# Kernel tuning notes

Hardware: AMD Instinct MI355X
Metric: run time of the kernel (lower is better)

## Reference

```python
import jax, jax.numpy as jnp
import numpy as np

N, E, IN_C, H, C1, OUT_C, B = 10000, 100000, 256, 6, 128, 128, 64
EPS = 1e-5
NEG_SLOPE = 0.2


def gat_conv(x, src, dst, W, att_s, att_d, bias):
    # x: [N, F_in]; W: [F_in, H*C]; att_s/att_d: [H, C]; bias: [H*C]
    n, h, c = x.shape[0], att_s.shape[0], att_s.shape[1]
    hx = (x @ W).reshape(n, h, c)                    # [N,H,C]
    a_s = jnp.einsum('nhc,hc->nh', hx, att_s)        # [N,H]
    a_d = jnp.einsum('nhc,hc->nh', hx, att_d)
    e = jax.nn.leaky_relu(a_s[src] + a_d[dst], NEG_SLOPE)   # [E,H]
    # segment softmax over incoming edges of each dst node
    m = jax.ops.segment_max(e, dst, num_segments=n)
    e = jnp.exp(e - m[dst])
    s = jax.ops.segment_sum(e, dst, num_segments=n)
    alpha = e / s[dst]                               # [E,H]
    msg = hx[src] * alpha[:, :, None]                # [E,H,C]
    out = jax.ops.segment_sum(msg, dst, num_segments=n)
    return out.reshape(n, h * c) + bias


def batch_norm(x, gamma, beta):
    mu = jnp.mean(x, axis=0)
    var = jnp.var(x, axis=0)  # biased, as torch BN uses for normalization
    return (x - mu) * jax.lax.rsqrt(var + EPS) * gamma + beta


def setup_inputs() -> dict:
    key = jax.random.key(0)
    ks = jax.random.split(key, 12)
    def xavier(k, shape):
        fan_in, fan_out = shape[0], shape[1]
        lim = np.sqrt(6.0 / (fan_in + fan_out))
        return jax.random.uniform(k, shape, jnp.float32, -lim, lim)
    inp = {}
    inp['input_feature'] = jax.random.normal(ks[0], (N, IN_C), jnp.float32)
    inp['input_adj'] = jax.random.randint(ks[1], (2, E), 0, N, jnp.int64)
    inp['ibatch'] = (jnp.arange(N, dtype=jnp.int64) * B) // N  # sorted graph ids, all B graphs covered
    # conv1: in -> H*C1
    inp['W1'] = xavier(ks[2], (IN_C, H * C1))
    inp['att_s1'] = xavier(ks[3], (H, C1)) * 0.1
    inp['att_d1'] = xavier(ks[4], (H, C1)) * 0.1
    inp['b1'] = jnp.zeros((H * C1,), jnp.float32)
    inp['g1'] = jnp.ones((H * C1,), jnp.float32)
    inp['be1'] = jnp.zeros((H * C1,), jnp.float32)
    # conv2: H*C1 -> H*OUT_C
    inp['W2'] = xavier(ks[5], (H * C1, H * OUT_C))
    inp['att_s2'] = xavier(ks[6], (H, OUT_C)) * 0.1
    inp['att_d2'] = xavier(ks[7], (H, OUT_C)) * 0.1
    inp['b2'] = jnp.zeros((H * OUT_C,), jnp.float32)
    inp['g2'] = jnp.ones((H * OUT_C,), jnp.float32)
    inp['be2'] = jnp.zeros((H * OUT_C,), jnp.float32)
    # gcn_linear: H*OUT_C -> OUT_C
    inp['lin_W'] = xavier(ks[8], (H * OUT_C, OUT_C))
    inp['lin_b'] = jnp.zeros((OUT_C,), jnp.float32)
    return inp


def reference(input_feature, input_adj, ibatch, W1, att_s1, att_d1, b1, g1, be1,
              W2, att_s2, att_d2, b2, g2, be2, lin_W, lin_b):
    # add self loops (PyG GATConv default)
    loops = jnp.arange(N, dtype=input_adj.dtype)
    src = jnp.concatenate([input_adj[0], loops])
    dst = jnp.concatenate([input_adj[1], loops])
    x = gat_conv(input_feature, src, dst, W1, att_s1, att_d1, b1)
    x = batch_norm(jax.nn.relu(x), g1, be1)
    x = gat_conv(x, src, dst, W2, att_s2, att_d2, b2)
    x = batch_norm(jax.nn.relu(x), g2, be2)
    x = x @ lin_W + lin_b                             # [N, OUT_C]
    # global max pool over nodes of each graph
    return jax.ops.segment_max(x, ibatch, num_segments=B)
```

## Files before the change

kernel.cpp:

```cpp
#include <hip/hip_runtime.h>

#define NN 10000
#define MP 10112
#define EE 100000
#define ETOT 110000
#define INC 256
#define HH 6
#define CC 128
#define FF 768
#define BB 64
#define BN_EPS 1e-5f

typedef unsigned short ushort_t;
typedef unsigned int uint_t;
typedef __attribute__((ext_vector_type(8))) short bf16x8;
typedef __attribute__((ext_vector_type(4))) float f32x4;
#define AS1 __attribute__((address_space(1)))
#define AS3 __attribute__((address_space(3)))

__device__ __forceinline__ unsigned fenc(float v){
  unsigned u = __float_as_uint(v);
  return (u & 0x80000000u) ? ~u : (u | 0x80000000u);
}
__device__ __forceinline__ float fdec(unsigned u){
  return (u & 0x80000000u) ? __uint_as_float(u & 0x7FFFFFFFu) : __uint_as_float(~u);
}

__device__ __forceinline__ ushort_t f2bf(float v){
  unsigned u = __float_as_uint(v);
  u += 0x7FFFu + ((u >> 16) & 1u);
  return (ushort_t)(u >> 16);
}
__device__ __forceinline__ float bf_lo(uint_t u){ return __uint_as_float(u << 16); }
__device__ __forceinline__ float bf_hi(uint_t u){ return __uint_as_float(u & 0xFFFF0000u); }

__device__ __forceinline__ float bn_scale(const float* sums, const float* sumsq,
                                          const float* g, int k){
  float mu  = sums[k] * (1.f/NN);
  float var = sumsq[k] * (1.f/NN) - mu*mu;
  return g[k] * rsqrtf(var + BN_EPS);
}

#define PREP_CNT 430
#define PREP_TR  (24*8)
#define PREP_CVT 2500
__global__ __launch_bounds__(256) void prep(const int* __restrict__ adj, int* __restrict__ deg,
                                            const float* __restrict__ W1, ushort_t* __restrict__ W1t,
                                            const float* __restrict__ feat, ushort_t* __restrict__ featB){
  __shared__ ushort_t tile[32][33];
  int bid = blockIdx.x, tid = threadIdx.x;
  if(bid < PREP_CNT){
    int k = bid*256 + tid;
    if(k < ETOT){
      int d = (k < EE) ? adj[EE + k] : (k - EE);
      atomicAdd(deg + d, 1);
    }
  } else if(bid < PREP_CNT + PREP_TR){
    int b = bid - PREP_CNT;
    int nb = (b % 24)*32, kb = (b / 24)*32;
    int tx = tid & 31, ty = tid >> 5;
    #pragma unroll
    for(int r = ty; r < 32; r += 8)
      tile[tx][r] = f2bf(W1[(size_t)(kb + r)*FF + nb + tx]);
    __syncthreads();
    #pragma unroll
    for(int r = ty; r < 32; r += 8)
      W1t[(size_t)(nb + r)*INC + kb + tx] = tile[r][tx];
  } else {
    int i = (bid - PREP_CNT - PREP_TR)*256 + tid;
    float4 v = ((const float4*)feat)[i];
    ushort4 o;
    o.x = f2bf(v.x); o.y = f2bf(v.y); o.z = f2bf(v.z); o.w = f2bf(v.w);
    ((ushort4*)featB)[i] = o;
  }
}

__global__ __launch_bounds__(1024) void scan_deg(const int* __restrict__ deg,
                                                 int* __restrict__ row_start,
                                                 int* __restrict__ pos){
  __shared__ int wsum[16];
  __shared__ int wexcl[16];
  __shared__ int carry, ctot;
  int t = threadIdx.x, wave = t >> 6, lane = t & 63;
  if(t == 0) carry = 0;
  __syncthreads();
  for(int base = 0; base < NN; base += 1024){
    int i = base + t;
    int v = (i < NN) ? deg[i] : 0;
    int s = v;
    #pragma unroll
    for(int off = 1; off < 64; off <<= 1){ int x = __shfl_up(s, off); if(lane >= off) s += x; }
    if(lane == 63) wsum[wave] = s;
    __syncthreads();
    if(t < 16){
      int ws = wsum[t], sc = ws;
      #pragma unroll
      for(int off = 1; off < 16; off <<= 1){ int x = __shfl_up(sc, off); if(t >= off) sc += x; }
      wexcl[t] = sc - ws;
      if(t == 15) ctot = sc;
    }
    __syncthreads();
    int c = carry;
    if(i < NN){ int excl = c + wexcl[wave] + s - v; row_start[i] = excl; pos[i] = excl; }
    __syncthreads();
    if(t == 0) carry = c + ctot;
  }
  __syncthreads();
  if(t == 0) row_start[NN] = carry;
}

__global__ __launch_bounds__(256) void scatter_edges(const int* __restrict__ adj,
                                                     int* __restrict__ pos,
                                                     int* __restrict__ csr_src){
  int k = blockIdx.x*256 + threadIdx.x;
  if(k >= ETOT) return;
  int s, d;
  if(k < EE){ s = adj[k]; d = adj[EE + k]; } else { s = k - EE; d = s; }
  int i = atomicAdd(pos + d, 1);
  csr_src[i] = s;
}

__global__ __launch_bounds__(256) void wfold(const float* __restrict__ W,
                                             int K, int N,
                                             const float* __restrict__ sums,
                                             const float* __restrict__ sumsq,
                                             const float* __restrict__ g,
                                             const float* __restrict__ be,
                                             const float* __restrict__ base,
                                             ushort_t* __restrict__ Wt,
                                             float* __restrict__ biasOut){
  __shared__ ushort_t tile[32][33];
  int nT = (K >> 5)*(N >> 5);
  int bid = blockIdx.x, tid = threadIdx.x;
  if(bid < nT){
    int nb = (bid % (N >> 5))*32, kb = (bid / (N >> 5))*32;
    int tx = tid & 31, ty = tid >> 5;
    #pragma unroll
    for(int r = ty; r < 32; r += 8){
      int k = kb + r;
      tile[tx][r] = f2bf(W[(size_t)k*N + nb + tx] * bn_scale(sums, sumsq, g, k));
    }
    __syncthreads();
    #pragma unroll
    for(int r = ty; r < 32; r += 8)
      Wt[(size_t)(nb + r)*K + kb + tx] = tile[r][tx];
  } else {
    int b = bid - nT;
    int oChunks = (N + 255) >> 8;
    int kc = b / oChunks, oc = b % oChunks;
    int o = oc*256 + tid;
    if(o >= N) return;
    int k0 = kc*64, k1 = k0 + 64;
    float s = 0.f;
    for(int k = k0; k < k1; k++){
      float mu = sums[k] * (1.f/NN);
      float sc = bn_scale(sums, sumsq, g, k);
      s = fmaf(be[k] - mu*sc, W[(size_t)k*N + o], s);
    }
    if(k0 == 0 && base) s += base[o];
    atomicAdd(biasOut + o, s);
  }
}

#define CTS 136
__global__ __launch_bounds__(256) void gemm_bt(const ushort_t* __restrict__ A,
                                               const ushort_t* __restrict__ Bt,
                                               ushort_t* __restrict__ Cb,
                                               int M, int N, int K,
                                               const float* __restrict__ bias,
                                               const float* __restrict__ atts,
                                               const float* __restrict__ attd,
                                               float* __restrict__ a_s,
                                               float* __restrict__ a_d,
                                               const int* __restrict__ ibatch,
                                               unsigned* __restrict__ outEnc){
  __shared__ ushort_t smem[8704];
  __shared__ unsigned smax[2*CC];
  __shared__ int s_split;
  ushort_t* As = smem;
  ushort_t* Bs = smem + 4096;
  int tid = threadIdx.x;
  int bm = blockIdx.y*128, bn = blockIdx.x*128;
  int w = tid >> 6, lane = tid & 63;
  int wr = (w >> 1)*64, wc = (w & 1)*64;
  int quad = lane >> 4, l15 = lane & 15;

  f32x4 acc[4][4];
  #pragma unroll
  for(int i=0;i<4;i++)
    #pragma unroll
    for(int j=0;j<4;j++) acc[i][j] = (f32x4){0.f,0.f,0.f,0.f};

  int ch0 = tid, ch1 = tid + 256;
  int ar0 = ch0 >> 2, ac0 = (ch0 & 3) << 3;
  int ar1 = ch1 >> 2, ac1 = (ch1 & 3) << 3;
  const ushort_t* Ag0 = A + (size_t)(bm + ar0)*K + ac0;
  const ushort_t* Ag1 = A + (size_t)(bm + ar1)*K + ac1;
  const ushort_t* Bg0 = Bt + (size_t)(bn + ar0)*K + ac0;
  const ushort_t* Bg1 = Bt + (size_t)(bn + ar1)*K + ac1;

  for(int k0 = 0; k0 < K; k0 += 32){
    __builtin_amdgcn_global_load_lds((const AS1 uint_t*)(Ag0 + k0),
                                     (AS3 uint_t*)(As + ch0*8), 16, 0, 0);
    __builtin_amdgcn_global_load_lds((const AS1 uint_t*)(Ag1 + k0),
                                     (AS3 uint_t*)(As + ch1*8), 16, 0, 0);
    __builtin_amdgcn_global_load_lds((const AS1 uint_t*)(Bg0 + k0),
                                     (AS3 uint_t*)(Bs + ch0*8), 16, 0, 0);
    __builtin_amdgcn_global_load_lds((const AS1 uint_t*)(Bg1 + k0),
                                     (AS3 uint_t*)(Bs + ch1*8), 16, 0, 0);
    __syncthreads();

    bf16x8 a[4], b[4];
    #pragma unroll
    for(int i=0;i<4;i++) a[i] = *(const bf16x8*)&As[(wr + i*16 + l15)*32 + quad*8];
    #pragma unroll
    for(int j=0;j<4;j++) b[j] = *(const bf16x8*)&Bs[(wc + j*16 + l15)*32 + quad*8];
    #pragma unroll
    for(int i=0;i<4;i++)
      #pragma unroll
      for(int j=0;j<4;j++)
        acc[i][j] = __builtin_amdgcn_mfma_f32_16x16x32_bf16(a[i], b[j], acc[i][j], 0, 0, 0);
    __syncthreads();
  }

  int h = bn >> 7;
  float bv4[4];
  #pragma unroll
  for(int j=0;j<4;j++){
    int gc = bn + wc + j*16 + l15;
    bv4[j] = bias ? bias[gc] : 0.f;
  }

  if(outEnc){
    if(tid == 0) s_split = bm + 128;
    for(int q = tid; q < 2*CC; q += 256) smax[q] = 0u;
    __syncthreads();
    if(tid < 127){
      int r1 = bm + tid + 1;
      if(r1 < M && ibatch[r1] != ibatch[r1 - 1]) s_split = r1;
    }
    __syncthreads();
    int gsplit = s_split;
    float pm[2][4];
    #pragma unroll
    for(int s2=0;s2<2;s2++)
      #pragma unroll
      for(int j=0;j<4;j++) pm[s2][j] = -__builtin_inff();
    #pragma unroll
    for(int i=0;i<4;i++){
      #pragma unroll
      for(int r=0;r<4;r++){
        int gr = bm + wr + i*16 + quad*4 + r;
        if(gr < M){
          int slot = (gr >= gsplit);
          #pragma unroll
          for(int j=0;j<4;j++)
            pm[slot][j] = fmaxf(pm[slot][j], acc[i][j][r] + bv4[j]);
        }
      }
    }
    #pragma unroll
    for(int s2=0;s2<2;s2++)
      #pragma unroll
      for(int j=0;j<4;j++){
        if(pm[s2][j] > -__builtin_inff())
          atomicMax(&smax[s2*CC + wc + j*16 + l15], fenc(pm[s2][j]));
      }
    __syncthreads();
    if(tid < 2*CC){
      unsigned v = smax[tid];
      if(v){
        int slot = tid >> 7, c = tid & 127;
        int g = ibatch[slot ? gsplit : bm];
        atomicMax(outEnc + g*CC + c, v);
      }
    }
  } else {
    ushort_t* Ct = smem;
    int myp = w >> 1;
    #pragma unroll
    for(int p=0;p<2;p++){
      if(myp == p){
        #pragma unroll
        for(int i=0;i<4;i++)
          #pragma unroll
          for(int r=0;r<4;r++){
            int row = i*16 + quad*4 + r;
            #pragma unroll
            for(int j=0;j<4;j++)
              Ct[row*CTS + wc + j*16 + l15] = f2bf(acc[i][j][r] + bv4[j]);
          }
      }
      __syncthreads();
      #pragma unroll
      for(int k=0;k<4;k++){
        int c = tid + 256*k;
        int row = c >> 4, o16 = c & 15;
        int gr = bm + p*64 + row;
        if(gr < M)
          *(uint4*)(Cb + (size_t)gr*N + bn + o16*8) = *(const uint4*)&Ct[row*CTS + o16*8];
      }
      if(atts){
        int row = tid >> 2, qtr = tid & 3;
        int gr = bm + p*64 + row;
        float sp = 0.f, dp = 0.f;
        const float2* asp = (const float2*)(atts + h*CC) + qtr*16;
        const float2* adp = (const float2*)(attd + h*CC) + qtr*16;
        const uint_t* cr = (const uint_t*)smem + ((row*CTS) >> 1) + qtr*16;
        #pragma unroll
        for(int c2=0;c2<16;c2++){
          uint_t u = cr[c2];
          float2 a2 = asp[c2], d2 = adp[c2];
          sp = fmaf(bf_lo(u), a2.x, fmaf(bf_hi(u), a2.y, sp));
          dp = fmaf(bf_lo(u), d2.x, fmaf(bf_hi(u), d2.y, dp));
        }
        sp += __shfl_xor(sp, 1); sp += __shfl_xor(sp, 2);
        dp += __shfl_xor(dp, 1); dp += __shfl_xor(dp, 2);
        if(qtr == 0 && gr < M){ a_s[gr*6 + h] = sp; a_d[gr*6 + h] = dp; }
      }
      __syncthreads();
    }
  }
}

__global__ __launch_bounds__(384) void aggregate(const ushort_t* __restrict__ hx,
                                                 const float* __restrict__ a_s,
                                                 const float* __restrict__ a_d,
                                                 const int* __restrict__ row_start,
                                                 const int* __restrict__ csr_src,
                                                 const float* __restrict__ bias,
                                                 ushort_t* __restrict__ y){
  int n = blockIdx.x, t = threadIdx.x, h = t >> 6;
  int e0 = row_start[n], e1 = row_start[n+1];
  float adv = a_d[n*6 + h];
  float a0 = 0.f, a1 = 0.f, wsum = 0.f;
  int i = e0;
  for(; i + 8 <= e1; i += 8){
    int s[8]; float wv[8]; uint_t u[8];
    #pragma unroll
    for(int q=0;q<8;q++) s[q] = csr_src[i+q];
    #pragma unroll
    for(int q=0;q<8;q++) wv[q] = a_s[s[q]*6 + h];
    #pragma unroll
    for(int q=0;q<8;q++) u[q] = ((const uint_t*)(hx + (size_t)s[q]*FF))[t];
    #pragma unroll
    for(int q=0;q<8;q++){
      float v = wv[q] + adv;
      v = v > 0.f ? v : 0.2f * v;
      float wq = __expf(v);
      wsum += wq;
      a0 = fmaf(wq, bf_lo(u[q]), a0); a1 = fmaf(wq, bf_hi(u[q]), a1);
    }
  }
  if(i + 4 <= e1){
    int s[4]; float wv[4]; uint_t u[4];
    #pragma unroll
    for(int q=0;q<4;q++) s[q] = csr_src[i+q];
    #pragma unroll
    for(int q=0;q<4;q++) wv[q] = a_s[s[q]*6 + h];
    #pragma unroll
    for(int q=0;q<4;q++) u[q] = ((const uint_t*)(hx + (size_t)s[q]*FF))[t];
    #pragma unroll
    for(int q=0;q<4;q++){
      float v = wv[q] + adv;
      v = v > 0.f ? v : 0.2f * v;
      float wq = __expf(v);
      wsum += wq;
      a0 = fmaf(wq, bf_lo(u[q]), a0); a1 = fmaf(wq, bf_hi(u[q]), a1);
    }
    i += 4;
  }
  for(; i < e1; i++){
    int s = csr_src[i];
    float v = a_s[s*6 + h] + adv;
    v = v > 0.f ? v : 0.2f * v;
    float wq = __expf(v);
    wsum += wq;
    uint_t u = ((const uint_t*)(hx + (size_t)s*FF))[t];
    a0 = fmaf(wq, bf_lo(u), a0); a1 = fmaf(wq, bf_hi(u), a1);
  }
  float inv = 1.f/wsum;
  float2 bv = ((const float2*)bias)[t];
  float v0 = a0*inv + bv.x;
  float v1 = a1*inv + bv.y;
  v0 = v0 > 0.f ? v0 : 0.f;
  v1 = v1 > 0.f ? v1 : 0.f;
  uint_t p = (uint_t)f2bf(v0) | ((uint_t)f2bf(v1) << 16);
  ((uint_t*)(y + (size_t)n*FF))[t] = p;
}

__global__ __launch_bounds__(384) void bn_stats(const ushort_t* __restrict__ y,
                                                float* __restrict__ sums,
                                                float* __restrict__ sumsq){
  int t = threadIdx.x;
  float s0=0.f,s1=0.f,q0=0.f,q1=0.f;
  for(int n = blockIdx.x; n < NN; n += gridDim.x){
    uint_t u = ((const uint_t*)(y + (size_t)n*FF))[t];
    float lo = bf_lo(u), hi = bf_hi(u);
    s0 += lo; q0 += lo*lo;
    s1 += hi; q1 += hi*hi;
  }
  atomicAdd(sums + 2*t,     s0); atomicAdd(sumsq + 2*t,     q0);
  atomicAdd(sums + 2*t + 1, s1); atomicAdd(sumsq + 2*t + 1, q1);
}

__global__ __launch_bounds__(256) void decode_out(const unsigned* __restrict__ outEnc,
                                                  float* __restrict__ out){
  int i = blockIdx.x*256 + threadIdx.x;
  if(i < BB*CC) out[i] = fdec(outEnc[i]);
}

extern "C" void kernel_launch(void* const* d_in, const int* in_sizes, int n_in,
                              void* d_out, int out_size, void* d_ws, size_t ws_size,
                              hipStream_t stream){
  const float* feat  = (const float*)d_in[0];
  const int*   adj   = (const int*)d_in[1];
  const int*   ibatch= (const int*)d_in[2];
  const float* W1    = (const float*)d_in[3];
  const float* atts1 = (const float*)d_in[4];
  const float* attd1 = (const float*)d_in[5];
  const float* b1    = (const float*)d_in[6];
  const float* g1    = (const float*)d_in[7];
  const float* be1   = (const float*)d_in[8];
  const float* W2    = (const float*)d_in[9];
  const float* atts2 = (const float*)d_in[10];
  const float* attd2 = (const float*)d_in[11];
  const float* b2    = (const float*)d_in[12];
  const float* g2    = (const float*)d_in[13];
  const float* be2   = (const float*)d_in[14];
  const float* linW  = (const float*)d_in[15];
  const float* linb  = (const float*)d_in[16];
  float* out = (float*)d_out;

  size_t off = 0;
  auto alloc = [&](size_t bytes) -> void* {
    void* p = (char*)d_ws + off;
    off += (bytes + 255) & ~(size_t)255;
    return p;
  };
  size_t zoff0 = off;
  int*      deg     = (int*)alloc((size_t)NN*4);
  float*    sumsA   = (float*)alloc((size_t)2*FF*4);
  float*    sumsB   = (float*)alloc((size_t)2*FF*4);
  float*    bias2p  = (float*)alloc((size_t)FF*4);
  float*    biasLp  = (float*)alloc((size_t)CC*4);
  unsigned* outEnc  = (unsigned*)alloc((size_t)BB*CC*4);
  size_t zbytes = off - zoff0;
  ushort_t* hx      = (ushort_t*)alloc((size_t)NN*FF*2);
  ushort_t* yB      = (ushort_t*)alloc((size_t)MP*FF*2);
  ushort_t* featB   = (ushort_t*)alloc((size_t)MP*INC*2);
  ushort_t* W1t     = (ushort_t*)alloc((size_t)FF*INC*2);
  ushort_t* W2t     = (ushort_t*)alloc((size_t)FF*FF*2);
  ushort_t* linWt   = (ushort_t*)alloc((size_t)CC*FF*2);
  float*    a_s     = (float*)alloc((size_t)NN*6*4);
  float*    a_d     = (float*)alloc((size_t)NN*6*4);
  int*      row_start=(int*)alloc((size_t)(NN+1)*4);
  int*      pos     = (int*)alloc((size_t)NN*4);
  int*      csr_src = (int*)alloc((size_t)ETOT*4);

  const int EB = (ETOT + 255)/256;

  hipMemsetAsync((char*)d_ws + zoff0, 0, zbytes, stream);

  prep<<<PREP_CNT + PREP_TR + PREP_CVT,256,0,stream>>>(adj, deg, W1, W1t, feat, featB);
  scan_deg<<<1,1024,0,stream>>>(deg, row_start, pos);
  scatter_edges<<<EB,256,0,stream>>>(adj, pos, csr_src);

  gemm_bt<<<dim3(FF/128, MP/128),256,0,stream>>>(featB, W1t, hx, NN, FF, INC,
                                                 nullptr, atts1, attd1, a_s, a_d, nullptr, nullptr);
  aggregate<<<NN,384,0,stream>>>(hx, a_s, a_d, row_start, csr_src, b1, yB);
  bn_stats<<<256,384,0,stream>>>(yB, sumsA, sumsA + FF);

  wfold<<<(FF/32)*(FF/32) + (FF/64)*3,256,0,stream>>>(W2, FF, FF, sumsA, sumsA + FF, g1, be1,
                                                      nullptr, W2t, bias2p);
  gemm_bt<<<dim3(FF/128, MP/128),256,0,stream>>>(yB, W2t, hx, NN, FF, FF,
                                                 bias2p, atts2, attd2, a_s, a_d, nullptr, nullptr);
  aggregate<<<NN,384,0,stream>>>(hx, a_s, a_d, row_start, csr_src, b2, yB);
  bn_stats<<<256,384,0,stream>>>(yB, sumsB, sumsB + FF);

  wfold<<<(FF/32)*(CC/32) + (FF/64)*1,256,0,stream>>>(linW, FF, CC, sumsB, sumsB + FF, g2, be2,
                                                      linb, linWt, biasLp);
  gemm_bt<<<dim3(CC/128, MP/128),256,0,stream>>>(yB, linWt, nullptr, NN, CC, FF,
                                                 biasLp, nullptr, nullptr, nullptr, nullptr,
                                                 ibatch, outEnc);
  decode_out<<<(BB*CC+255)/256,256,0,stream>>>(outEnc, out);
}
```

Before: 327.1 us.

## Split-K the final linear GEMM and move max-pooling into a separate kernel

The final linear layer (N x 768 by 768 x 128) used to launch only 79 blocks with fused max-pool. It now runs a split-K GEMM with 4 K-chunks and 64-row tiles (632 blocks), writing fp32 partial sums to a workspace. A new pool kernel then sums the partials, adds the bias and does the per-graph segment max with atomics. This aims to fill more CUs, at the cost of an extra launch and about 20 MB of partial-sum writes and reads.

```diff
diff --git a/kernel.cpp b/kernel.cpp
--- a/kernel.cpp
+++ b/kernel.cpp
@@ -171,12 +171,8 @@
                                                const float* __restrict__ atts,
                                                const float* __restrict__ attd,
                                                float* __restrict__ a_s,
-                                               float* __restrict__ a_d,
-                                               const int* __restrict__ ibatch,
-                                               unsigned* __restrict__ outEnc){
+                                               float* __restrict__ a_d){
   __shared__ ushort_t smem[8704];
-  __shared__ unsigned smax[2*CC];
-  __shared__ int s_split;
   ushort_t* As = smem;
   ushort_t* Bs = smem + 4096;
   int tid = threadIdx.x;
@@ -230,97 +226,133 @@
     int gc = bn + wc + j*16 + l15;
     bv4[j] = bias ? bias[gc] : 0.f;
   }
-
-  if(outEnc){
-    if(tid == 0) s_split = bm + 128;
-    for(int q = tid; q < 2*CC; q += 256) smax[q] = 0u;
-    __syncthreads();
-    if(tid < 127){
-      int r1 = bm + tid + 1;
-      if(r1 < M && ibatch[r1] != ibatch[r1 - 1]) s_split = r1;
-    }
-    __syncthreads();
-    int gsplit = s_split;
-    float pm[2][4];
-    #pragma unroll
-    for(int s2=0;s2<2;s2++)
+  ushort_t* Ct = smem;
+  int myp = w >> 1;
+  #pragma unroll
+  for(int p=0;p<2;p++){
+    if(myp == p){
       #pragma unroll
-      for(int j=0;j<4;j++) pm[s2][j] = -__builtin_inff();
-    #pragma unroll
-    for(int i=0;i<4;i++){
-      #pragma unroll
-      for(int r=0;r<4;r++){
-        int gr = bm + wr + i*16 + quad*4 + r;
-        if(gr < M){
-          int slot = (gr >= gsplit);
+      for(int i=0;i<4;i++)
+        #pragma unroll
+        for(int r=0;r<4;r++){
+          int row = i*16 + quad*4 + r;
           #pragma unroll
           for(int j=0;j<4;j++)
-            pm[slot][j] = fmaxf(pm[slot][j], acc[i][j][r] + bv4[j]);
+            Ct[row*CTS + wc + j*16 + l15] = f2bf(acc[i][j][r] + bv4[j]);
         }
+    }
+    __syncthreads();
+    #pragma unroll
+    for(int k=0;k<4;k++){
+      int c = tid + 256*k;
+      int row = c >> 4, o16 = c & 15;
+      int gr = bm + p*64 + row;
+      if(gr < M)
+        *(uint4*)(Cb + (size_t)gr*N + bn + o16*8) = *(const uint4*)&Ct[row*CTS + o16*8];
+    }
+    if(atts){
+      int row = tid >> 2, qtr = tid & 3;
+      int gr = bm + p*64 + row;
+      float sp = 0.f, dp = 0.f;
+      const float2* asp = (const float2*)(atts + h*CC) + qtr*16;
+      const float2* adp = (const float2*)(attd + h*CC) + qtr*16;
+      const uint_t* cr = (const uint_t*)smem + ((row*CTS) >> 1) + qtr*16;
+      #pragma unroll
+      for(int c2=0;c2<16;c2++){
+        uint_t u = cr[c2];
+        float2 a2 = asp[c2], d2 = adp[c2];
+        sp = fmaf(bf_lo(u), a2.x, fmaf(bf_hi(u), a2.y, sp));
+        dp = fmaf(bf_lo(u), d2.x, fmaf(bf_hi(u), d2.y, dp));
       }
-    }
-    #pragma unroll
-    for(int s2=0;s2<2;s2++)
+      sp += __shfl_xor(sp, 1); sp += __shfl_xor(sp, 2);
+      dp += __shfl_xor(dp, 1); dp += __shfl_xor(dp, 2);
+      if(qtr == 0 && gr < M){ a_s[gr*6 + h] = sp; a_d[gr*6 + h] = dp; }
+    }
+    __syncthreads();
+  }
+}
+
+#define KS 4
+#define KCH 192
+__global__ __launch_bounds__(256) void gemmL(const ushort_t* __restrict__ A,
+                                             const ushort_t* __restrict__ Bt,
+                                             float* __restrict__ zs){
+  __shared__ ushort_t As[64*32];
+  __shared__ ushort_t Bs[128*32];
+  int tid = threadIdx.x;
+  int kc0 = blockIdx.x*KCH;
+  int bm = blockIdx.y*64;
+  int w = tid >> 6, lane = tid & 63;
+  int wr = (w >> 1)*32, wc = (w & 1)*64;
+  int quad = lane >> 4, l15 = lane & 15;
+
+  f32x4 acc[2][4];
+  #pragma unroll
+  for(int i=0;i<2;i++)
+    #pragma unroll
+    for(int j=0;j<4;j++) acc[i][j] = (f32x4){0.f,0.f,0.f,0.f};
+
+  int ch0 = tid, ch1 = tid + 256;
+  const ushort_t* Ag  = A  + (size_t)(bm + (ch0 >> 2))*FF + kc0 + ((ch0 & 3) << 3);
+  const ushort_t* Bg0 = Bt + (size_t)(ch0 >> 2)*FF + kc0 + ((ch0 & 3) << 3);
+  const ushort_t* Bg1 = Bt + (size_t)(ch1 >> 2)*FF + kc0 + ((ch1 & 3) << 3);
+
+  for(int k0 = 0; k0 < KCH; k0 += 32){
+    __builtin_amdgcn_global_load_lds((const AS1 uint_t*)(Ag + k0),
+                                     (AS3 uint_t*)(As + ch0*8), 16, 0, 0);
+    __builtin_amdgcn_global_load_lds((const AS1 uint_t*)(Bg0 + k0),
+                                     (AS3 uint_t*)(Bs + ch0*8), 16, 0, 0);
+    __builtin_amdgcn_global_load_lds((const AS1 uint_t*)(Bg1 + k0),
+                                     (AS3 uint_t*)(Bs + ch1*8), 16, 0, 0);
+    __syncthreads();
+    bf16x8 a[2], b[4];
+    #pragma unroll
+    for(int i=0;i<2;i++) a[i] = *(const bf16x8*)&As[(wr + i*16 + l15)*32 + quad*8];
+    #pragma unroll
+    for(int j=0;j<4;j++) b[j] = *(const bf16x8*)&Bs[(wc + j*16 + l15)*32 + quad*8];
+    #pragma unroll
+    for(int i=0;i<2;i++)
       #pragma unroll
-      for(int j=0;j<4;j++){
-        if(pm[s2][j] > -__builtin_inff())
-          atomicMax(&smax[s2*CC + wc + j*16 + l15], fenc(pm[s2][j]));
-      }
-    __syncthreads();
-    if(tid < 2*CC){
-      unsigned v = smax[tid];
-      if(v){
-        int slot = tid >> 7, c = tid & 127;
-        int g = ibatch[slot ? gsplit : bm];
-        atomicMax(outEnc + g*CC + c, v);
-      }
-    }
-  } else {
-    ushort_t* Ct = smem;
-    int myp = w >> 1;
-    #pragma unroll
-    for(int p=0;p<2;p++){
-      if(myp == p){
-        #pragma unroll
-        for(int i=0;i<4;i++)
-          #pragma unroll
-          for(int r=0;r<4;r++){
-            int row = i*16 + quad*4 + r;
-            #pragma unroll
-            for(int j=0;j<4;j++)
-              Ct[row*CTS + wc + j*16 + l15] = f2bf(acc[i][j][r] + bv4[j]);
-          }
-      }
-      __syncthreads();
+      for(int j=0;j<4;j++)
+        acc[i][j] = __builtin_amdgcn_mfma_f32_16x16x32_bf16(a[i], b[j], acc[i][j], 0, 0, 0);
+    __syncthreads();
+  }
+
+  float* zp = zs + ((size_t)blockIdx.x*MP + bm)*CC;
+  #pragma unroll
+  for(int i=0;i<2;i++)
+    #pragma unroll
+    for(int r=0;r<4;r++){
+      int row = wr + i*16 + quad*4 + r;
       #pragma unroll
-      for(int k=0;k<4;k++){
-        int c = tid + 256*k;
-        int row = c >> 4, o16 = c & 15;
-        int gr = bm + p*64 + row;
-        if(gr < M)
-          *(uint4*)(Cb + (size_t)gr*N + bn + o16*8) = *(const uint4*)&Ct[row*CTS + o16*8];
-      }
-      if(atts){
-        int row = tid >> 2, qtr = tid & 3;
-        int gr = bm + p*64 + row;
-        float sp = 0.f, dp = 0.f;
-        const float2* asp = (const float2*)(atts + h*CC) + qtr*16;
-        const float2* adp = (const float2*)(attd + h*CC) + qtr*16;
-        const uint_t* cr = (const uint_t*)smem + ((row*CTS) >> 1) + qtr*16;
-        #pragma unroll
-        for(int c2=0;c2<16;c2++){
-          uint_t u = cr[c2];
-          float2 a2 = asp[c2], d2 = adp[c2];
-          sp = fmaf(bf_lo(u), a2.x, fmaf(bf_hi(u), a2.y, sp));
-          dp = fmaf(bf_lo(u), d2.x, fmaf(bf_hi(u), d2.y, dp));
-        }
-        sp += __shfl_xor(sp, 1); sp += __shfl_xor(sp, 2);
-        dp += __shfl_xor(dp, 1); dp += __shfl_xor(dp, 2);
-        if(qtr == 0 && gr < M){ a_s[gr*6 + h] = sp; a_d[gr*6 + h] = dp; }
-      }
-      __syncthreads();
-    }
-  }
+      for(int j=0;j<4;j++)
+        zp[row*CC + wc + j*16 + l15] = acc[i][j][r];
+    }
+}
+
+__global__ __launch_bounds__(128) void poolz(const float* __restrict__ zs,
+                                             const float* __restrict__ bias,
+                                             const int* __restrict__ ibatch,
+                                             unsigned* __restrict__ outEnc){
+  int c = threadIdx.x;
+  int r0 = blockIdx.x*128;
+  int r1 = r0 + 128; if(r1 > NN) r1 = NN;
+  if(r0 >= NN) return;
+  float bv = bias[c];
+  const float* z0 = zs;
+  const float* z1 = zs + (size_t)MP*CC;
+  const float* z2 = zs + (size_t)2*MP*CC;
+  const float* z3 = zs + (size_t)3*MP*CC;
+  int g = ibatch[r0];
+  float m = -__builtin_inff();
+  for(int r = r0; r < r1; r++){
+    size_t o = (size_t)r*CC + c;
+    float v = z0[o] + z1[o] + z2[o] + z3[o] + bv;
+    int gr = ibatch[r];
+    if(gr != g){ atomicMax(outEnc + g*CC + c, fenc(m)); g = gr; m = -__builtin_inff(); }
+    m = fmaxf(m, v);
+  }
+  atomicMax(outEnc + g*CC + c, fenc(m));
 }
 
 __global__ __launch_bounds__(384) void aggregate(const ushort_t* __restrict__ hx,
@@ -452,6 +484,7 @@
   ushort_t* W1t     = (ushort_t*)alloc((size_t)FF*INC*2);
   ushort_t* W2t     = (ushort_t*)alloc((size_t)FF*FF*2);
   ushort_t* linWt   = (ushort_t*)alloc((size_t)CC*FF*2);
+  float*    zs      = (float*)alloc((size_t)KS*MP*CC*4);
   float*    a_s     = (float*)alloc((size_t)NN*6*4);
   float*    a_d     = (float*)alloc((size_t)NN*6*4);
   int*      row_start=(int*)alloc((size_t)(NN+1)*4);
@@ -467,21 +500,20 @@
   scatter_edges<<<EB,256,0,stream>>>(adj, pos, csr_src);
 
   gemm_bt<<<dim3(FF/128, MP/128),256,0,stream>>>(featB, W1t, hx, NN, FF, INC,
-                                                 nullptr, atts1, attd1, a_s, a_d, nullptr, nullptr);
+                                                 nullptr, atts1, attd1, a_s, a_d);
   aggregate<<<NN,384,0,stream>>>(hx, a_s, a_d, row_start, csr_src, b1, yB);
   bn_stats<<<256,384,0,stream>>>(yB, sumsA, sumsA + FF);
 
   wfold<<<(FF/32)*(FF/32) + (FF/64)*3,256,0,stream>>>(W2, FF, FF, sumsA, sumsA + FF, g1, be1,
                                                       nullptr, W2t, bias2p);
   gemm_bt<<<dim3(FF/128, MP/128),256,0,stream>>>(yB, W2t, hx, NN, FF, FF,
-                                                 bias2p, atts2, attd2, a_s, a_d, nullptr, nullptr);
+                                                 bias2p, atts2, attd2, a_s, a_d);
   aggregate<<<NN,384,0,stream>>>(hx, a_s, a_d, row_start, csr_src, b2, yB);
   bn_stats<<<256,384,0,stream>>>(yB, sumsB, sumsB + FF);
 
   wfold<<<(FF/32)*(CC/32) + (FF/64)*1,256,0,stream>>>(linW, FF, CC, sumsB, sumsB + FF, g2, be2,
                                                       linb, linWt, biasLp);
-  gemm_bt<<<dim3(CC/128, MP/128),256,0,stream>>>(yB, linWt, nullptr, NN, CC, FF,
-                                                 biasLp, nullptr, nullptr, nullptr, nullptr,
-                                                 ibatch, outEnc);
+  gemmL<<<dim3(KS, MP/64),256,0,stream>>>(yB, linWt, zs);
+  poolz<<<(NN+127)/128,128,0,stream>>>(zs, biasLp, ibatch, outEnc);
   decode_out<<<(BB*CC+255)/256,256,0,stream>>>(outEnc, out);
 }
```

Result: slower. 358.2 us (+9.5%).
